# Performance work log

Hardware: AMD Instinct MI355X
Metric: run time of the kernel (lower is better)

The kernel has to match this reference:

```python
import jax, jax.numpy as jnp
import numpy as np

N = 524288   # total points across all events
H = 128      # MLP hidden width
B = 1024     # number of batches (events)


def setup_inputs() -> dict:
    key = jax.random.key(0)
    ks = jax.random.split(key, 6)
    # features[:,0] = per-point input mean, features[:,1] = per-point input std (>0)
    mean = jax.random.normal(ks[0], (N, 1), dtype=jnp.float32)
    std = jax.random.uniform(ks[1], (N, 1), dtype=jnp.float32) * 0.5 + 0.1
    features = jnp.concatenate([mean, std], axis=1)            # [N,2]
    batch_ids = jax.random.randint(ks[2], (N,), 0, B).astype(jnp.int32)
    s = 1.0 / np.sqrt(H).astype(np.float32)
    W1 = jax.random.normal(ks[3], (1, H), dtype=jnp.float32)
    b1 = jnp.zeros((H,), jnp.float32)
    W2 = jax.random.normal(ks[4], (H, H), dtype=jnp.float32) * s
    b2 = jnp.zeros((H,), jnp.float32)
    W3 = jax.random.normal(ks[5], (H, 1), dtype=jnp.float32) * s
    b3 = jnp.zeros((1,), jnp.float32)
    return {"features": features, "batch_ids": batch_ids,
            "W1": W1, "b1": b1, "W2": W2, "b2": b2, "W3": W3, "b3": b3,
            "num_batches": B}


def reference(features, batch_ids, W1, b1, W2, b2, W3, b3, num_batches):
    x0 = features[:, :1]        # [N,1] input means (x.features in the original)
    inpt_std = features[:, 1]   # [N]   input stds
    n = x0.shape[0]
    counts = jnp.maximum(
        jax.ops.segment_sum(jnp.ones((n,), x0.dtype), batch_ids,
                            num_segments=num_batches), 1.0)      # [B]

    def net(x):
        # pointwise MLP then global average pool per batch -> one scalar per event
        h = jnp.tanh(x @ W1 + b1)        # [N,H]
        h = jnp.tanh(h @ W2 + b2)        # [N,H]
        s = (h @ W3 + b3)[:, 0]          # [N]
        return jax.ops.segment_sum(s, batch_ids, num_segments=num_batches) / counts  # [B]

    pred_mean, vjp_fn = jax.vjp(net, x0)
    # d pred[b] / d x_j is nonzero only for points j in batch b (pointwise net +
    # per-batch pool), so ONE VJP with a ones cotangent yields every per-batch
    # Jacobian row simultaneously -- collapsing the original per-batch
    # torch.autograd.grad loop into a single backward pass.
    jac = vjp_fn(jnp.ones_like(pred_mean))[0][:, 0]              # [N]
    # var_b = jac_b^T diag(std_b^2) jac_b = sum_{j in b} std_j^2 * jac_j^2
    pred_sdp_var = jax.ops.segment_sum(inpt_std ** 2 * jac ** 2, batch_ids,
                                       num_segments=num_batches)  # [B]
    return jnp.stack([pred_mean, pred_sdp_var], axis=1)           # [B,2]
```

## Files before the change

### kernel.cpp

```cpp
#include <hip/hip_runtime.h>


#define HH   128
#define NB   1024
#define TBL  4096
#define XMIN (-8.0f)
#define XMAX (8.0f)
#define EPB  16
#define BUILD_BLOCKS (TBL / EPB)
#define MAIN_BLOCKS  256

__global__ __launch_bounds__(256) void build_table_kernel(
    const float* __restrict__ W1, const float* __restrict__ b1,
    const float* __restrict__ W2, const float* __restrict__ b2,
    const float* __restrict__ W3, const float* __restrict__ b3,
    float2* __restrict__ tab2, float* __restrict__ acc, unsigned* __restrict__ done)
{
    __shared__ float W2s[HH * HH];
    __shared__ float hus[HH * 2 * EPB];
    const int tid = threadIdx.x;
    {
        const float4* src = (const float4*)W2;
        float4* dst = (float4*)W2s;
        for (int i = tid; i < HH * HH / 4; i += 256) dst[i] = src[i];
    }
    if (blockIdx.x == 0) {
        for (int i = tid; i < 3 * NB; i += 256) acc[i] = 0.0f;
        if (tid == 0) *done = 0u;
    }
    const float dxt = (XMAX - XMIN) / (float)(TBL - 1);
    const int ebase = blockIdx.x * EPB;
    for (int i = tid; i < EPB * HH; i += 256) {
        int e = i & (EPB - 1);
        int k = i >> 4;
        float x = XMIN + (float)(ebase + e) * dxt;
        float w1 = W1[k];
        float h = tanhf(fmaf(x, w1, b1[k]));
        hus[k * (2 * EPB) + 2 * e]     = h;
        hus[k * (2 * EPB) + 2 * e + 1] = w1 * (1.0f - h * h);
    }
    __syncthreads();

    const int q = tid & 31;
    const int r = tid >> 5;
    const int jb = q * 4;
    float z0[4] = {0,0,0,0}, v0[4] = {0,0,0,0};
    float z1[4] = {0,0,0,0}, v1[4] = {0,0,0,0};
    #pragma unroll 4
    for (int k = 0; k < HH; ++k) {
        float4 w  = *(const float4*)&W2s[k * HH + jb];
        float4 hu = *(const float4*)&hus[k * (2 * EPB) + 4 * r];
        z0[0] = fmaf(hu.x, w.x, z0[0]); z0[1] = fmaf(hu.x, w.y, z0[1]);
        z0[2] = fmaf(hu.x, w.z, z0[2]); z0[3] = fmaf(hu.x, w.w, z0[3]);
        v0[0] = fmaf(hu.y, w.x, v0[0]); v0[1] = fmaf(hu.y, w.y, v0[1]);
        v0[2] = fmaf(hu.y, w.z, v0[2]); v0[3] = fmaf(hu.y, w.w, v0[3]);
        z1[0] = fmaf(hu.z, w.x, z1[0]); z1[1] = fmaf(hu.z, w.y, z1[1]);
        z1[2] = fmaf(hu.z, w.z, z1[2]); z1[3] = fmaf(hu.z, w.w, z1[3]);
        v1[0] = fmaf(hu.w, w.x, v1[0]); v1[1] = fmaf(hu.w, w.y, v1[1]);
        v1[2] = fmaf(hu.w, w.z, v1[2]); v1[3] = fmaf(hu.w, w.w, v1[3]);
    }
    float ps0 = 0.f, pd0 = 0.f, ps1 = 0.f, pd1 = 0.f;
    #pragma unroll
    for (int i = 0; i < 4; ++i) {
        int j = jb + i;
        float b2j = b2[j], w3 = W3[j];
        float h2 = tanhf(z0[i] + b2j);
        ps0 = fmaf(w3, h2, ps0);
        pd0 = fmaf((1.0f - h2 * h2) * w3, v0[i], pd0);
        float h2b = tanhf(z1[i] + b2j);
        ps1 = fmaf(w3, h2b, ps1);
        pd1 = fmaf((1.0f - h2b * h2b) * w3, v1[i], pd1);
    }
    #pragma unroll
    for (int o = 16; o > 0; o >>= 1) {
        ps0 += __shfl_down(ps0, o, 32); pd0 += __shfl_down(pd0, o, 32);
        ps1 += __shfl_down(ps1, o, 32); pd1 += __shfl_down(pd1, o, 32);
    }
    if (q == 0) {
        float bb = b3[0];
        int e = ebase + 2 * r;
        tab2[e]     = make_float2(ps0 + bb, pd0);
        tab2[e + 1] = make_float2(ps1 + bb, pd1);
    }
}

__device__ __forceinline__ float cm(float fm, float f0, float f1, float f2, float t) {
    float a1 = 0.5f * (f1 - fm);
    float a2 = fm - 2.5f * f0 + 2.0f * f1 - 0.5f * f2;
    float a3 = 1.5f * (f0 - f1) + 0.5f * (f2 - fm);
    return fmaf(fmaf(fmaf(a3, t, a2), t, a1), t, f0);
}

__global__ __launch_bounds__(256) void main_pass_kernel(
    const float2* __restrict__ feat, const int* __restrict__ ids,
    const float2* __restrict__ tab2, float* __restrict__ acc,
    unsigned* __restrict__ done, float* __restrict__ out, int n)
{
    __shared__ float bs[NB];
    __shared__ float bv[NB];
    __shared__ float bc[NB];
    __shared__ int lastflag;
    const int tid = threadIdx.x;
    for (int i = tid; i < NB; i += 256) { bs[i] = 0.f; bv[i] = 0.f; bc[i] = 0.f; }
    __syncthreads();
    const float inv_dx = (float)(TBL - 1) / (XMAX - XMIN);
    const int stride = MAIN_BLOCKS * 256;
    for (int i = blockIdx.x * 256 + tid; i < n; i += stride) {
        float2 f = feat[i];
        int b = ids[i];
        float u = (fminf(fmaxf(f.x, XMIN), XMAX) - XMIN) * inv_dx;
        int i0 = (int)u;
        i0 = min(max(i0, 1), TBL - 3);
        float t = u - (float)i0;
        float2 fm = tab2[i0 - 1], f0 = tab2[i0], f1 = tab2[i0 + 1], f2 = tab2[i0 + 2];
        float s = cm(fm.x, f0.x, f1.x, f2.x, t);
        float d = cm(fm.y, f0.y, f1.y, f2.y, t);
        atomicAdd(&bs[b], s);
        atomicAdd(&bv[b], f.y * f.y * d * d);
        atomicAdd(&bc[b], 1.0f);
    }
    __syncthreads();
    for (int b = tid; b < NB; b += 256) {
        float c = bc[b];
        if (c != 0.f) {
            atomicAdd(&acc[b], bs[b]);
            atomicAdd(&acc[NB + b], bv[b]);
            atomicAdd(&acc[2 * NB + b], c);
        }
    }
    __threadfence();
    __syncthreads();
    if (tid == 0) {
        unsigned old = __hip_atomic_fetch_add(done, 1u, __ATOMIC_ACQ_REL,
                                              __HIP_MEMORY_SCOPE_AGENT);
        lastflag = (old == (unsigned)(MAIN_BLOCKS - 1)) ? 1 : 0;
    }
    __syncthreads();
    if (lastflag) {
        for (int b = tid; b < NB; b += 256) {
            float ssum = __hip_atomic_load(&acc[b], __ATOMIC_RELAXED,
                                           __HIP_MEMORY_SCOPE_AGENT);
            float vsum = __hip_atomic_load(&acc[NB + b], __ATOMIC_RELAXED,
                                           __HIP_MEMORY_SCOPE_AGENT);
            float c = __hip_atomic_load(&acc[2 * NB + b], __ATOMIC_RELAXED,
                                        __HIP_MEMORY_SCOPE_AGENT);
            c = fmaxf(c, 1.0f);
            out[2 * b]     = ssum / c;
            out[2 * b + 1] = vsum / (c * c);
        }
    }
}

extern "C" void kernel_launch(void* const* d_in, const int* in_sizes, int n_in,
                              void* d_out, int out_size, void* d_ws, size_t ws_size,
                              hipStream_t stream) {
    const float* feat = (const float*)d_in[0];
    const int*   ids  = (const int*)d_in[1];
    const float* W1   = (const float*)d_in[2];
    const float* b1   = (const float*)d_in[3];
    const float* W2   = (const float*)d_in[4];
    const float* b2   = (const float*)d_in[5];
    const float* W3   = (const float*)d_in[6];
    const float* b3   = (const float*)d_in[7];
    const int n = in_sizes[1];

    float2*   tab2 = (float2*)d_ws;
    float*    acc  = (float*)(tab2 + TBL);
    unsigned* done = (unsigned*)(acc + 3 * NB);

    build_table_kernel<<<BUILD_BLOCKS, 256, 0, stream>>>(W1, b1, W2, b2, W3, b3,
                                                         tab2, acc, done);
    main_pass_kernel<<<MAIN_BLOCKS, 256, 0, stream>>>((const float2*)feat, ids,
                                                      tab2, acc, done,
                                                      (float*)d_out, n);
}
```

Measured before the change: 116.3 us.

## Stage split interpolation tables in LDS and finalize in a separate kernel

Splits the interleaved float2 table into separate value and derivative arrays and copies both into shared memory at the start of each main-pass block, so the four-point Catmull-Rom lookups read LDS instead of global/L2 memory. The interpolation is recast as per-point weights applied to both tables. The last-block-done atomic counter and fence are replaced by a small third kernel that normalizes the accumulated sums. This adds 32 KB of LDS per block and an extra kernel launch.

```diff
diff --git a/kernel.cpp b/kernel.cpp
--- a/kernel.cpp
+++ b/kernel.cpp
@@ -14,7 +14,8 @@
     const float* __restrict__ W1, const float* __restrict__ b1,
     const float* __restrict__ W2, const float* __restrict__ b2,
     const float* __restrict__ W3, const float* __restrict__ b3,
-    float2* __restrict__ tab2, float* __restrict__ acc, unsigned* __restrict__ done)
+    float* __restrict__ s_tab, float* __restrict__ d_tab,
+    float* __restrict__ acc)
 {
     __shared__ float W2s[HH * HH];
     __shared__ float hus[HH * 2 * EPB];
@@ -26,7 +27,6 @@
     }
     if (blockIdx.x == 0) {
         for (int i = tid; i < 3 * NB; i += 256) acc[i] = 0.0f;
-        if (tid == 0) *done = 0u;
     }
     const float dxt = (XMAX - XMIN) / (float)(TBL - 1);
     const int ebase = blockIdx.x * EPB;
@@ -79,28 +79,29 @@
     if (q == 0) {
         float bb = b3[0];
         int e = ebase + 2 * r;
-        tab2[e]     = make_float2(ps0 + bb, pd0);
-        tab2[e + 1] = make_float2(ps1 + bb, pd1);
+        s_tab[e]     = ps0 + bb;  d_tab[e]     = pd0;
+        s_tab[e + 1] = ps1 + bb;  d_tab[e + 1] = pd1;
     }
-}
-
-__device__ __forceinline__ float cm(float fm, float f0, float f1, float f2, float t) {
-    float a1 = 0.5f * (f1 - fm);
-    float a2 = fm - 2.5f * f0 + 2.0f * f1 - 0.5f * f2;
-    float a3 = 1.5f * (f0 - f1) + 0.5f * (f2 - fm);
-    return fmaf(fmaf(fmaf(a3, t, a2), t, a1), t, f0);
 }
 
 __global__ __launch_bounds__(256) void main_pass_kernel(
     const float2* __restrict__ feat, const int* __restrict__ ids,
-    const float2* __restrict__ tab2, float* __restrict__ acc,
-    unsigned* __restrict__ done, float* __restrict__ out, int n)
+    const float* __restrict__ s_tab, const float* __restrict__ d_tab,
+    float* __restrict__ acc, int n)
 {
+    __shared__ float ts[TBL];
+    __shared__ float td[TBL];
     __shared__ float bs[NB];
     __shared__ float bv[NB];
     __shared__ float bc[NB];
-    __shared__ int lastflag;
     const int tid = threadIdx.x;
+    {
+        const float4* s4 = (const float4*)s_tab;
+        const float4* d4 = (const float4*)d_tab;
+        float4* t4 = (float4*)ts;
+        float4* u4 = (float4*)td;
+        for (int i = tid; i < TBL / 4; i += 256) { t4[i] = s4[i]; u4[i] = d4[i]; }
+    }
     for (int i = tid; i < NB; i += 256) { bs[i] = 0.f; bv[i] = 0.f; bc[i] = 0.f; }
     __syncthreads();
     const float inv_dx = (float)(TBL - 1) / (XMAX - XMIN);
@@ -112,9 +113,13 @@
         int i0 = (int)u;
         i0 = min(max(i0, 1), TBL - 3);
         float t = u - (float)i0;
-        float2 fm = tab2[i0 - 1], f0 = tab2[i0], f1 = tab2[i0 + 1], f2 = tab2[i0 + 2];
-        float s = cm(fm.x, f0.x, f1.x, f2.x, t);
-        float d = cm(fm.y, f0.y, f1.y, f2.y, t);
+        float t2 = t * t, t3 = t2 * t;
+        float wm = -0.5f * t3 + t2 - 0.5f * t;
+        float w0 =  1.5f * t3 - 2.5f * t2 + 1.0f;
+        float w1 = -1.5f * t3 + 2.0f * t2 + 0.5f * t;
+        float w2 =  0.5f * t3 - 0.5f * t2;
+        float s = wm * ts[i0 - 1] + w0 * ts[i0] + w1 * ts[i0 + 1] + w2 * ts[i0 + 2];
+        float d = wm * td[i0 - 1] + w0 * td[i0] + w1 * td[i0 + 1] + w2 * td[i0 + 2];
         atomicAdd(&bs[b], s);
         atomicAdd(&bv[b], f.y * f.y * d * d);
         atomicAdd(&bc[b], 1.0f);
@@ -128,26 +133,15 @@
             atomicAdd(&acc[2 * NB + b], c);
         }
     }
-    __threadfence();
-    __syncthreads();
-    if (tid == 0) {
-        unsigned old = __hip_atomic_fetch_add(done, 1u, __ATOMIC_ACQ_REL,
-                                              __HIP_MEMORY_SCOPE_AGENT);
-        lastflag = (old == (unsigned)(MAIN_BLOCKS - 1)) ? 1 : 0;
-    }
-    __syncthreads();
-    if (lastflag) {
-        for (int b = tid; b < NB; b += 256) {
-            float ssum = __hip_atomic_load(&acc[b], __ATOMIC_RELAXED,
-                                           __HIP_MEMORY_SCOPE_AGENT);
-            float vsum = __hip_atomic_load(&acc[NB + b], __ATOMIC_RELAXED,
-                                           __HIP_MEMORY_SCOPE_AGENT);
-            float c = __hip_atomic_load(&acc[2 * NB + b], __ATOMIC_RELAXED,
-                                        __HIP_MEMORY_SCOPE_AGENT);
-            c = fmaxf(c, 1.0f);
-            out[2 * b]     = ssum / c;
-            out[2 * b + 1] = vsum / (c * c);
-        }
+}
+
+__global__ __launch_bounds__(256) void finalize_kernel(const float* __restrict__ acc,
+                                                       float* __restrict__ out) {
+    int b = blockIdx.x * 256 + threadIdx.x;
+    if (b < NB) {
+        float c = fmaxf(acc[2 * NB + b], 1.0f);
+        out[2 * b]     = acc[b] / c;
+        out[2 * b + 1] = acc[NB + b] / (c * c);
     }
 }
 
@@ -164,13 +158,13 @@
     const float* b3   = (const float*)d_in[7];
     const int n = in_sizes[1];
 
-    float2*   tab2 = (float2*)d_ws;
-    float*    acc  = (float*)(tab2 + TBL);
-    unsigned* done = (unsigned*)(acc + 3 * NB);
+    float* s_tab = (float*)d_ws;
+    float* d_tab = s_tab + TBL;
+    float* acc   = d_tab + TBL;
 
     build_table_kernel<<<BUILD_BLOCKS, 256, 0, stream>>>(W1, b1, W2, b2, W3, b3,
-                                                         tab2, acc, done);
+                                                         s_tab, d_tab, acc);
     main_pass_kernel<<<MAIN_BLOCKS, 256, 0, stream>>>((const float2*)feat, ids,
-                                                      tab2, acc, done,
-                                                      (float*)d_out, n);
+                                                      s_tab, d_tab, acc, n);
+    finalize_kernel<<<(NB + 255) / 256, 256, 0, stream>>>(acc, (float*)d_out);
 }
```

Measured after the change: 101.8 us. -12.5%, faster.
